# Kernel tuning notes

Hardware: AMD Instinct MI355X
Metric: run time of the kernel (lower is better)

Reference implementation:

```python
import jax, jax.numpy as jnp
import numpy as np

M = 16          # num_particles
EPS = 0.006


def setup_inputs() -> dict:
    key = jax.random.key(0)
    k1, k2, k3, k4 = jax.random.split(key, 4)
    B, P, O = 131072, 16, 4  # batch, pred_horizon, obs_horizon
    return {
        "ys_t": jax.random.normal(k1, (B, P, O), dtype=jnp.float32),
        "ys_r_stop": jax.random.normal(k2, (B, P, O), dtype=jnp.float32),
        "w_scale": jax.random.uniform(k3, (B,), dtype=jnp.float32),
        "time_weights": jax.random.uniform(k4, (B,), dtype=jnp.float32),
    }


def _laplace(a, b, ws, D):
    # a,b: [G, M, D]; ws: [G, M] (scale indexed by j, the first particle index)
    d = jnp.linalg.norm(a[:, :, None, :] - b[:, None, :, :], axis=-1)  # [G, M, M]
    d = jnp.maximum(d, EPS)
    return jnp.exp(-ws[:, :, None] * d / D)


def reference(ys_t, ys_r_stop, w_scale, time_weights):
    B = ys_t.shape[0]
    G = B // M
    x = ys_t.reshape(G, M, -1)        # [G, M, D]
    y = ys_r_stop.reshape(G, M, -1)   # [G, M, D]
    D = x.shape[-1]                   # pred_horizon * obs_horizon (dim_normalize)
    ws = w_scale.reshape(G, M)
    tw = time_weights.reshape(G, M)[:, 0]  # [G]
    terms = _laplace(x, x, ws, D) + _laplace(y, y, ws, D) - 2.0 * _laplace(x, y, ws, D)
    group_loss = terms.sum(axis=(1, 2)) * tw / (M * M)  # [G]
    return group_loss.sum() / G
```

## Files before the change

kernel.cpp:

```cpp
#include <hip/hip_runtime.h>


#define EPS_D 0.006f
#define DIMS 64

__global__ __launch_bounds__(256, 2)
void imm_loss_kernel(const float* __restrict__ ys_t,
                     const float* __restrict__ ys_r,
                     const float* __restrict__ w_scale,
                     const float* __restrict__ time_w,
                     float* __restrict__ partials)
{
    const int tid  = threadIdx.x;
    const int lane = tid & 63;
    const int wave = tid >> 6;
    const int j    = lane & 15;
    const int b    = (blockIdx.x * 4 + wave) * 64 + lane;

    float x[DIMS], y[DIMS];
    const float4* xp = reinterpret_cast<const float4*>(ys_t + (size_t)b * DIMS);
    const float4* yp = reinterpret_cast<const float4*>(ys_r + (size_t)b * DIMS);
    #pragma unroll
    for (int c = 0; c < DIMS / 4; ++c) {
        float4 v = xp[c];
        x[4*c+0] = v.x; x[4*c+1] = v.y; x[4*c+2] = v.z; x[4*c+3] = v.w;
    }
    #pragma unroll
    for (int c = 0; c < DIMS / 4; ++c) {
        float4 v = yp[c];
        y[4*c+0] = v.x; y[4*c+1] = v.y; y[4*c+2] = v.z; y[4*c+3] = v.w;
    }

    const float s_j = w_scale[b] * (1.0f / (float)DIMS);
    const float tw  = time_w[b & ~15];

    float acc = 2.0f * __expf(-s_j * EPS_D);

    {
        float d2 = 0.f;
        #pragma unroll
        for (int d = 0; d < DIMS; ++d) {
            float t = x[d] - y[d];
            d2 = fmaf(t, t, d2);
        }
        float dd = fmaxf(sqrtf(d2), EPS_D);
        acc -= 2.0f * __expf(-s_j * dd);
    }

    const int clbase = lane & 48;

    for (int o = 1; o <= 8; ++o) {
        const int src = clbase | ((j + o) & 15);
        const float s_k = __shfl(s_j, src, 64);
        float dxx = 0.f, dyy = 0.f, dxy = 0.f;
        #pragma unroll
        for (int d = 0; d < DIMS; ++d) {
            float xr = __shfl(x[d], src, 64);
            float yr = __shfl(y[d], src, 64);
            float tx = x[d] - xr;  dxx = fmaf(tx, tx, dxx);
            float ty = y[d] - yr;  dyy = fmaf(ty, ty, dyy);
            float tz = x[d] - yr;  dxy = fmaf(tz, tz, dxy);
        }
        const float w   = (o == 8) ? 0.5f : 1.0f;
        const float ddx = fmaxf(sqrtf(dxx), EPS_D);
        const float ddy = fmaxf(sqrtf(dyy), EPS_D);
        const float ddz = fmaxf(sqrtf(dxy), EPS_D);
        acc += w * (__expf(-s_j * ddx) + __expf(-s_k * ddx));
        acc += w * (__expf(-s_j * ddy) + __expf(-s_k * ddy));
        acc -= 2.0f * __expf(-s_j * ddz);
    }

    for (int o = 9; o <= 15; ++o) {
        const int src = clbase | ((j + o) & 15);
        float dxy = 0.f;
        #pragma unroll
        for (int d = 0; d < DIMS; ++d) {
            float yr = __shfl(y[d], src, 64);
            float tz = x[d] - yr;
            dxy = fmaf(tz, tz, dxy);
        }
        const float ddz = fmaxf(sqrtf(dxy), EPS_D);
        acc -= 2.0f * __expf(-s_j * ddz);
    }

    float val = acc * tw;
    #pragma unroll
    for (int off = 32; off; off >>= 1)
        val += __shfl_xor(val, off, 64);

    __shared__ float smem[4];
    if (lane == 0) smem[wave] = val;
    __syncthreads();
    if (tid == 0)
        partials[blockIdx.x] = smem[0] + smem[1] + smem[2] + smem[3];
}

__global__ void imm_reduce_kernel(const float* __restrict__ part, int n,
                                  float inv_scale, float* __restrict__ out)
{
    const int tid = threadIdx.x;
    float v = 0.f;
    for (int i = tid; i < n; i += 256) v += part[i];
    #pragma unroll
    for (int off = 32; off; off >>= 1) v += __shfl_xor(v, off, 64);
    __shared__ float s[4];
    if ((tid & 63) == 0) s[tid >> 6] = v;
    __syncthreads();
    if (tid == 0) out[0] = (s[0] + s[1] + s[2] + s[3]) * inv_scale;
}

extern "C" void kernel_launch(void* const* d_in, const int* in_sizes, int n_in,
                              void* d_out, int out_size, void* d_ws, size_t ws_size,
                              hipStream_t stream)
{
    const float* ys_t = (const float*)d_in[0];
    const float* ys_r = (const float*)d_in[1];
    const float* wsc  = (const float*)d_in[2];
    const float* twp  = (const float*)d_in[3];
    float* out      = (float*)d_out;
    float* partials = (float*)d_ws;

    const int B = in_sizes[2];
    const int G = B / 16;
    const int blocks = G / 16;

    imm_loss_kernel<<<blocks, 256, 0, stream>>>(ys_t, ys_r, wsc, twp, partials);

    const float inv_scale = 1.0f / (256.0f * (float)G);
    imm_reduce_kernel<<<1, 256, 0, stream>>>(partials, blocks, inv_scale, out);
}
```

Baseline: 139.1 us.

## Split pair offsets across wave roles, use DPP row rotates, chunk dims

Each group of 64 particles is now handled by two waves. One wave computes offsets 1-5 plus the cross term at offset 9, and the other computes offsets 6-8, the self-diagonal cross term and offsets 10-15. Cross-lane fetches use DPP row_ror instead of ds_bpermute-based __shfl, which avoids LDS-path shuffles. The 64 dims are streamed in 16-element chunks, lowering register pressure so launch_bounds can rise to 4 blocks per CU and the grid doubles. The trade-off is that each input row is now loaded by two waves, and the two roles carry somewhat uneven work.

```diff
diff --git a/kernel.cpp b/kernel.cpp
--- a/kernel.cpp
+++ b/kernel.cpp
@@ -4,7 +4,40 @@
 #define EPS_D 0.006f
 #define DIMS 64
 
-__global__ __launch_bounds__(256, 2)
+#define ROT(v, O) __int_as_float(__builtin_amdgcn_update_dpp(              \
+        0, __float_as_int(v), 0x120 + (O), 0xF, 0xF, false))
+
+#define FULL_CH(O, I) {                                                    \
+    _Pragma("unroll")                                                      \
+    for (int d = 0; d < 16; ++d) {                                         \
+        float tx = ROT(xd[d], O) - xd[d];        \
+        float tz = ROT(yd[d], O) - xd[d];        \
+        float ty = tz + dl[d];                  \
+        fxx[I] = fmaf(tx, tx, fxx[I]);                                     \
+        fyy[I] = fmaf(ty, ty, fyy[I]);                                     \
+        fxy[I] = fmaf(tz, tz, fxy[I]);                                     \
+    } }
+
+#define XY_CH(O, I) {                                                      \
+    _Pragma("unroll")                                                      \
+    for (int d = 0; d < 16; ++d) {                                         \
+        float tz = ROT(yd[d], O) - xd[d];                                  \
+        gxy[I] = fmaf(tz, tz, gxy[I]);                                     \
+    } }
+
+#define EPI_FULL(O, I, W) {                                                \
+    const float s_k = ROT(s_j, O);                                         \
+    const float ddx = fmaxf(sqrtf(fxx[I]), EPS_D);                         \
+    const float ddy = fmaxf(sqrtf(fyy[I]), EPS_D);                         \
+    const float ddz = fmaxf(sqrtf(fxy[I]), EPS_D);                         \
+    acc += (W) * (__expf(-s_j * ddx) + __expf(-s_k * ddx));                \
+    acc += (W) * (__expf(-s_j * ddy) + __expf(-s_k * ddy));                \
+    acc -= 2.0f * __expf(-s_j * ddz); }
+
+#define EPI_XY(I)                                                          \
+    acc -= 2.0f * __expf(-s_j * fmaxf(sqrtf(gxy[I]), EPS_D));
+
+__global__ __launch_bounds__(256, 4)
 void imm_loss_kernel(const float* __restrict__ ys_t,
                      const float* __restrict__ ys_r,
                      const float* __restrict__ w_scale,
@@ -14,73 +47,59 @@
     const int tid  = threadIdx.x;
     const int lane = tid & 63;
     const int wave = tid >> 6;
-    const int j    = lane & 15;
-    const int b    = (blockIdx.x * 4 + wave) * 64 + lane;
+    const int role = wave & 1;
+    const int pair = wave >> 1;
+    const int b    = blockIdx.x * 128 + pair * 64 + lane;
 
-    float x[DIMS], y[DIMS];
-    const float4* xp = reinterpret_cast<const float4*>(ys_t + (size_t)b * DIMS);
-    const float4* yp = reinterpret_cast<const float4*>(ys_r + (size_t)b * DIMS);
-    #pragma unroll
-    for (int c = 0; c < DIMS / 4; ++c) {
-        float4 v = xp[c];
-        x[4*c+0] = v.x; x[4*c+1] = v.y; x[4*c+2] = v.z; x[4*c+3] = v.w;
-    }
-    #pragma unroll
-    for (int c = 0; c < DIMS / 4; ++c) {
-        float4 v = yp[c];
-        y[4*c+0] = v.x; y[4*c+1] = v.y; y[4*c+2] = v.z; y[4*c+3] = v.w;
-    }
+    const float* xrow = ys_t + (size_t)b * DIMS;
+    const float* yrow = ys_r + (size_t)b * DIMS;
 
     const float s_j = w_scale[b] * (1.0f / (float)DIMS);
     const float tw  = time_w[b & ~15];
 
-    float acc = 2.0f * __expf(-s_j * EPS_D);
+    float fxx[5] = {0,0,0,0,0}, fyy[5] = {0,0,0,0,0}, fxy[5] = {0,0,0,0,0};
+    float gxy[7] = {0,0,0,0,0,0,0};
 
-    {
-        float d2 = 0.f;
+    #pragma unroll
+    for (int c = 0; c < 4; ++c) {
+        float xd[16], yd[16], dl[16];
+        const float4* xp = reinterpret_cast<const float4*>(xrow + c * 16);
+        const float4* yp = reinterpret_cast<const float4*>(yrow + c * 16);
         #pragma unroll
-        for (int d = 0; d < DIMS; ++d) {
-            float t = x[d] - y[d];
-            d2 = fmaf(t, t, d2);
+        for (int q = 0; q < 4; ++q) {
+            float4 v = xp[q];
+            xd[4*q+0] = v.x; xd[4*q+1] = v.y; xd[4*q+2] = v.z; xd[4*q+3] = v.w;
         }
-        float dd = fmaxf(sqrtf(d2), EPS_D);
-        acc -= 2.0f * __expf(-s_j * dd);
+        #pragma unroll
+        for (int q = 0; q < 4; ++q) {
+            float4 v = yp[q];
+            yd[4*q+0] = v.x; yd[4*q+1] = v.y; yd[4*q+2] = v.z; yd[4*q+3] = v.w;
+        }
+        #pragma unroll
+        for (int d = 0; d < 16; ++d) dl[d] = xd[d] - yd[d];
+
+        if (role == 0) {
+            FULL_CH(1, 0) FULL_CH(2, 1) FULL_CH(3, 2) FULL_CH(4, 3) FULL_CH(5, 4)
+            XY_CH(9, 0)
+        } else {
+            FULL_CH(6, 0) FULL_CH(7, 1) FULL_CH(8, 2)
+            #pragma unroll
+            for (int d = 0; d < 16; ++d) gxy[0] = fmaf(dl[d], dl[d], gxy[0]);
+            XY_CH(10, 1) XY_CH(11, 2) XY_CH(12, 3)
+            XY_CH(13, 4) XY_CH(14, 5) XY_CH(15, 6)
+        }
     }
 
-    const int clbase = lane & 48;
-
-    for (int o = 1; o <= 8; ++o) {
-        const int src = clbase | ((j + o) & 15);
-        const float s_k = __shfl(s_j, src, 64);
-        float dxx = 0.f, dyy = 0.f, dxy = 0.f;
-        #pragma unroll
-        for (int d = 0; d < DIMS; ++d) {
-            float xr = __shfl(x[d], src, 64);
-            float yr = __shfl(y[d], src, 64);
-            float tx = x[d] - xr;  dxx = fmaf(tx, tx, dxx);
-            float ty = y[d] - yr;  dyy = fmaf(ty, ty, dyy);
-            float tz = x[d] - yr;  dxy = fmaf(tz, tz, dxy);
-        }
-        const float w   = (o == 8) ? 0.5f : 1.0f;
-        const float ddx = fmaxf(sqrtf(dxx), EPS_D);
-        const float ddy = fmaxf(sqrtf(dyy), EPS_D);
-        const float ddz = fmaxf(sqrtf(dxy), EPS_D);
-        acc += w * (__expf(-s_j * ddx) + __expf(-s_k * ddx));
-        acc += w * (__expf(-s_j * ddy) + __expf(-s_k * ddy));
-        acc -= 2.0f * __expf(-s_j * ddz);
-    }
-
-    for (int o = 9; o <= 15; ++o) {
-        const int src = clbase | ((j + o) & 15);
-        float dxy = 0.f;
-        #pragma unroll
-        for (int d = 0; d < DIMS; ++d) {
-            float yr = __shfl(y[d], src, 64);
-            float tz = x[d] - yr;
-            dxy = fmaf(tz, tz, dxy);
-        }
-        const float ddz = fmaxf(sqrtf(dxy), EPS_D);
-        acc -= 2.0f * __expf(-s_j * ddz);
+    float acc = 0.f;
+    if (role == 0) {
+        EPI_FULL(1, 0, 1.0f) EPI_FULL(2, 1, 1.0f) EPI_FULL(3, 2, 1.0f)
+        EPI_FULL(4, 3, 1.0f) EPI_FULL(5, 4, 1.0f)
+        EPI_XY(0)
+    } else {
+        EPI_FULL(6, 0, 1.0f) EPI_FULL(7, 1, 1.0f) EPI_FULL(8, 2, 0.5f)
+        acc += 2.0f * __expf(-s_j * EPS_D);
+        EPI_XY(0)
+        EPI_XY(1) EPI_XY(2) EPI_XY(3) EPI_XY(4) EPI_XY(5) EPI_XY(6)
     }
 
     float val = acc * tw;
@@ -122,7 +141,7 @@
 
     const int B = in_sizes[2];
     const int G = B / 16;
-    const int blocks = G / 16;
+    const int blocks = G / 8;
 
     imm_loss_kernel<<<blocks, 256, 0, stream>>>(ys_t, ys_r, wsc, twp, partials);
 
```

After: 220.6 us. +58.6%, slower.
